# Kernel tuning notes

Measured on AMD Instinct MI355X. Metric: run time of the kernel, lower is better.

## Reference

```python
import jax, jax.numpy as jnp
import numpy as np

OUT_H, OUT_W = 7, 7
SPATIAL_SCALE = 0.0625
SAMPLING_RATIO = 2  # fixed sampling grid (> 0 branch in the original)


def setup_inputs() -> dict:
    key = jax.random.key(0)
    k1, k2, k3, k4, k5 = jax.random.split(key, 5)
    B, C, H, W = 2, 256, 200, 200
    R = 512
    x = jax.random.normal(k1, (B, C, H, W), dtype=jnp.float32)
    img = W / SPATIAL_SCALE  # 3200 px image coordinates
    b = jax.random.randint(k2, (R,), 0, B).astype(jnp.float32)
    x1 = jax.random.uniform(k3, (R,), minval=0.0, maxval=img * 0.8)
    y1 = jax.random.uniform(k4, (R,), minval=0.0, maxval=img * 0.8)
    wh = jax.random.uniform(k5, (R, 2), minval=32.0, maxval=img * 0.2)
    rois = jnp.stack([b, x1, y1, x1 + wh[:, 0], y1 + wh[:, 1]], axis=1).astype(jnp.float32)
    return {"input": x, "rois": rois}


def _axis_coords(start, bin_size, pooled, sr):
    # start: [R]; returns sample coordinates [R, pooled*sr]
    p = jnp.arange(pooled, dtype=jnp.float32)
    i = jnp.arange(sr, dtype=jnp.float32)
    c = (start[:, None, None]
         + p[None, :, None] * bin_size[:, None, None]
         + (i[None, None, :] + 0.5) * bin_size[:, None, None] / sr)
    return c.reshape(start.shape[0], pooled * sr)


def _interp_axis(c, size):
    # per-axis bilinear pieces; c: [R, G]
    valid = (c >= -1.0) & (c <= size)
    cc = jnp.maximum(c, 0.0)
    lo = jnp.floor(cc)
    at_edge = lo >= size - 1
    lo_i = jnp.minimum(lo, size - 1).astype(jnp.int32)
    hi_i = jnp.minimum(lo_i + 1, size - 1)
    frac = jnp.where(at_edge, 0.0, cc - lo)  # l (weight toward hi)
    return lo_i, hi_i, frac, valid


def reference(input, rois):
    R = rois.shape[0]
    B, C, H, W = input.shape
    b = rois[:, 0].astype(jnp.int32)
    x1 = rois[:, 1] * SPATIAL_SCALE
    y1 = rois[:, 2] * SPATIAL_SCALE
    x2 = rois[:, 3] * SPATIAL_SCALE
    y2 = rois[:, 4] * SPATIAL_SCALE
    roi_w = jnp.maximum(x2 - x1, 1.0)
    roi_h = jnp.maximum(y2 - y1, 1.0)
    bin_w = roi_w / OUT_W
    bin_h = roi_h / OUT_H

    ys = _axis_coords(y1, bin_h, OUT_H, SAMPLING_RATIO)  # [R, Yg]
    xs = _axis_coords(x1, bin_w, OUT_W, SAMPLING_RATIO)  # [R, Xg]
    yl, yh, ly, vy = _interp_axis(ys, H)
    xl, xh, lx, vx = _interp_axis(xs, W)
    hy, hx = 1.0 - ly, 1.0 - lx

    bb = b[:, None, None]
    # advanced indexing -> [R, Yg, Xg, C]
    v1 = input[bb, :, yl[:, :, None], xl[:, None, :]]
    v2 = input[bb, :, yl[:, :, None], xh[:, None, :]]
    v3 = input[bb, :, yh[:, :, None], xl[:, None, :]]
    v4 = input[bb, :, yh[:, :, None], xh[:, None, :]]

    w1 = (hy[:, :, None] * hx[:, None, :])[..., None]
    w2 = (hy[:, :, None] * lx[:, None, :])[..., None]
    w3 = (ly[:, :, None] * hx[:, None, :])[..., None]
    w4 = (ly[:, :, None] * lx[:, None, :])[..., None]

    val = w1 * v1 + w2 * v2 + w3 * v3 + w4 * v4
    val = val * (vy[:, :, None] & vx[:, None, :])[..., None]

    S = SAMPLING_RATIO
    val = val.reshape(R, OUT_H, S, OUT_W, S, C).sum(axis=(2, 4)) / (S * S)
    return jnp.transpose(val, (0, 3, 1, 2))  # [R, C, OUT_H, OUT_W]
```

## Files before the change

### kernel.cpp

```cpp
#include <hip/hip_runtime.h>
#include <hip/hip_fp16.h>


#define B_  2
#define C_  256
#define H_  200
#define W_  200
#define R_  512
#define HW_ (H_ * W_)
#define TOTAL_ (B_ * C_ * HW_)
#define BUF_ 1600
#define G_   8

#define HDR_BYTES_  (R_ * 8 * 4)
#define META_BYTES_ (R_ * 4 * 64 * 16)
#define PERM_BYTES_ (R_ * 4)
#define WS_NEED_    (HDR_BYTES_ + META_BYTES_ + PERM_BYTES_)

typedef __attribute__((address_space(3))) unsigned int lds_u32;
typedef const __attribute__((address_space(1))) unsigned int glb_u32;

__device__ __forceinline__ float sample_coord(float start, float bin, int p, int i) {
    return start + (float)p * bin + ((float)i + 0.5f) * bin * 0.5f;
}
__device__ __forceinline__ int lo_clamped(float v, int size) {
    return (int)fminf(floorf(fmaxf(v, 0.0f)), (float)(size - 1));
}
__device__ __forceinline__ unsigned int pack_h2(float a, float b) {
    unsigned short ua = __half_as_ushort(__float2half(a));
    unsigned short ub = __half_as_ushort(__float2half(b));
    return (unsigned int)ua | ((unsigned int)ub << 16);
}
__device__ __forceinline__ float h2f_lo(unsigned int u) {
    return __half2float(__ushort_as_half((unsigned short)(u & 0xffffu)));
}
__device__ __forceinline__ float h2f_hi(unsigned int u) {
    return __half2float(__ushort_as_half((unsigned short)(u >> 16)));
}

__global__ __launch_bounds__(512) void roialign_sort(
    const float* __restrict__ rois, int* __restrict__ perm) {
    __shared__ unsigned int keys[R_];
    int t = threadIdx.x;

    float bf = rois[t * 5 + 0];
    float cx = (rois[t * 5 + 1] + rois[t * 5 + 3]) * 0.5f * 0.0625f;
    float cy = (rois[t * 5 + 2] + rois[t * 5 + 4]) * 0.5f * 0.0625f;
    int bi = (int)bf;
    int ys = min(3, max(0, (int)(cy * (4.0f / 200.0f))));
    int xq = min(255, max(0, (int)(cx * (256.0f / 200.0f))));
    unsigned int key = ((unsigned int)bi << 10) | ((unsigned int)ys << 8) |
                       (unsigned int)xq;
    unsigned int mykey = (key << 9) | (unsigned int)t;
    keys[t] = mykey;
    __syncthreads();

    int rank = 0;
#pragma unroll 8
    for (int u = 0; u < R_; ++u)
        rank += (keys[u] < mykey) ? 1 : 0;
    perm[rank] = t;
}

__global__ __launch_bounds__(64) void roialign_meta(
    const float* __restrict__ rois, int* __restrict__ hdr, int4* __restrict__ meta) {
    int r = blockIdx.x;
    int lane = threadIdx.x;

    const float scale = 0.0625f;
    float bf = rois[r * 5 + 0];
    int   bi = (int)bf;
    float x1 = rois[r * 5 + 1] * scale;
    float y1 = rois[r * 5 + 2] * scale;
    float x2 = rois[r * 5 + 3] * scale;
    float y2 = rois[r * 5 + 4] * scale;
    float bin_w = fmaxf(x2 - x1, 1.0f) * (1.0f / 7.0f);
    float bin_h = fmaxf(y2 - y1, 1.0f) * (1.0f / 7.0f);

    int y0 = lo_clamped(sample_coord(y1, bin_h, 0, 0), H_);
    int yE = min(lo_clamped(sample_coord(y1, bin_h, 6, 1), H_) + 1, H_ - 1);
    int x0 = lo_clamped(sample_coord(x1, bin_w, 0, 0), W_);
    int xE = min(lo_clamped(sample_coord(x1, bin_w, 6, 1), W_) + 1, W_ - 1);
    int rows = yE - y0 + 1;
    int cols = xE - x0 + 1;
    int cols4 = (cols + 3) & ~3;
    if ((cols4 & 31) == 0) cols4 += 4;
    int   T = rows * cols4;
    int   nIter = (T + 255) >> 8;
    float recip = 1.0f / (float)cols4;

    if (lane == 0) {
        int* h = hdr + r * 8;
        h[0] = y0 * W_ + x0;
        h[1] = bi;
        h[2] = cols4;
        h[3] = T;
        h[4] = __float_as_int(recip);
        h[5] = nIter;
        h[6] = 0;
        h[7] = 0;
    }

    int4 o[4] = {{0,0,0,0},{0,0,0,0},{0,0,0,0},{0,0,0,0}};
    if (lane < 49) {
        int ph = lane / 7;
        int pw = lane % 7;

        int   rlo_b[2], rhi_b[2];
        float fy[2];
        bool  vy[2];
#pragma unroll
        for (int iy = 0; iy < 2; ++iy) {
            float y = sample_coord(y1, bin_h, ph, iy);
            vy[iy] = (y >= -1.0f) && (y <= (float)H_);
            float yc = fmaxf(y, 0.0f);
            float yl = floorf(yc);
            bool  edge = yl >= (float)(H_ - 1);
            int   lo = (int)fminf(yl, (float)(H_ - 1));
            int   hi = min(lo + 1, H_ - 1);
            fy[iy] = edge ? 0.0f : (yc - yl);
            rlo_b[iy] = (lo - y0) * cols4 * 4;
            rhi_b[iy] = (hi - y0) * cols4 * 4;
        }
        int   clo_b[2], chi_b[2];
        float fx[2];
        bool  vx[2];
#pragma unroll
        for (int ix = 0; ix < 2; ++ix) {
            float x = sample_coord(x1, bin_w, pw, ix);
            vx[ix] = (x >= -1.0f) && (x <= (float)W_);
            float xc = fmaxf(x, 0.0f);
            float xl = floorf(xc);
            bool  edge = xl >= (float)(W_ - 1);
            int   lo = (int)fminf(xl, (float)(W_ - 1));
            int   hi = min(lo + 1, W_ - 1);
            fx[ix] = edge ? 0.0f : (xc - xl);
            clo_b[ix] = (lo - x0) * 4;
            chi_b[ix] = (hi - x0) * 4;
        }
#pragma unroll
        for (int iy = 0; iy < 2; ++iy)
#pragma unroll
            for (int ix = 0; ix < 2; ++ix) {
                int s = iy * 2 + ix;
                float mk  = (vy[iy] && vx[ix]) ? 0.25f : 0.0f;
                float wy0 = (1.0f - fy[iy]) * mk;
                float wy1 = fy[iy] * mk;
                float wx0 = 1.0f - fx[ix];
                float wx1 = fx[ix];
                o[s].x = rlo_b[iy] | (rhi_b[iy] << 16);
                o[s].y = clo_b[ix] | (chi_b[ix] << 16);
                o[s].z = (int)pack_h2(wy0, wy1);
                o[s].w = (int)pack_h2(wx0, wx1);
            }
    }
#pragma unroll
    for (int s = 0; s < 4; ++s)
        meta[((r * 4 + s) * 64) + lane] = o[s];
}

template<int N> __device__ __forceinline__ void wait_vmcnt() {
    if constexpr (N == 0)      asm volatile("s_waitcnt vmcnt(0)" ::: "memory");
    else if constexpr (N == 1) asm volatile("s_waitcnt vmcnt(1)" ::: "memory");
    else if constexpr (N == 2) asm volatile("s_waitcnt vmcnt(2)" ::: "memory");
    else if constexpr (N == 3) asm volatile("s_waitcnt vmcnt(3)" ::: "memory");
    else if constexpr (N == 4) asm volatile("s_waitcnt vmcnt(4)" ::: "memory");
    else if constexpr (N == 5) asm volatile("s_waitcnt vmcnt(5)" ::: "memory");
    else if constexpr (N == 6) asm volatile("s_waitcnt vmcnt(6)" ::: "memory");
    else                       asm volatile("s_waitcnt vmcnt(7)" ::: "memory");
}

template<int NI>
__device__ __forceinline__ void body(
    const float* __restrict__ input, float* __restrict__ out,
    float* __restrict__ b0, float* __restrict__ b1,
    int lane, int srcbase, int cols4, float recip, int T,
    const int (&off)[16], const float (&wt)[16], int obase) {

    int e4 = lane << 2;

    int so[NI];
#pragma unroll
    for (int i = 0; i < NI; ++i) {
        int e = e4 + (i << 8);
        int row = (int)(((float)e + 0.5f) * recip);
        int col = e - row * cols4;
        so[i] = srcbase + row * W_ + col;
    }

    auto STAGE = [&](float* bp) {
#pragma unroll
        for (int i = 0; i < NI; ++i) {
            if (e4 + (i << 8) < T) {
                int g = min(so[i], TOTAL_ - 4);
                __builtin_amdgcn_global_load_lds((glb_u32*)(input + g),
                                                 (lds_u32*)(bp + (i << 8)), 16, 0, 0);
            }
            so[i] += HW_;
        }
    };

    STAGE(b0);
    STAGE(b1);

    float accs[G_];
#pragma unroll
    for (int k = 0; k < G_; ++k) {
        if (k < G_ - 1) wait_vmcnt<NI>(); else wait_vmcnt<0>();
        float* bp = (k & 1) ? b1 : b0;
        const char* bb = (const char*)bp;
        float a = 0.0f;
#pragma unroll
        for (int s = 0; s < 4; ++s) {
            float v1 = *(const float*)(bb + off[4*s+0]);
            float v2 = *(const float*)(bb + off[4*s+1]);
            float v3 = *(const float*)(bb + off[4*s+2]);
            float v4 = *(const float*)(bb + off[4*s+3]);
            a += wt[4*s+0] * (wt[4*s+2] * v1 + wt[4*s+3] * v2)
               + wt[4*s+1] * (wt[4*s+2] * v3 + wt[4*s+3] * v4);
        }
        accs[k] = a;
        if (k < G_ - 2) {
            asm volatile("s_waitcnt lgkmcnt(0)" ::: "memory");
            __builtin_amdgcn_sched_barrier(0);
            STAGE(bp);
        }
    }

    if (lane < 49) {
#pragma unroll
        for (int k = 0; k < G_; ++k)
            out[obase + k * 49] = accs[k];
    }
}

__global__ __launch_bounds__(128) void roialign_main(
    const float* __restrict__ input, const int* __restrict__ hdr,
    const int4* __restrict__ meta, const int* __restrict__ perm,
    float* __restrict__ out) {
    __shared__ float lds[2][2][BUF_];
    int tid  = threadIdx.x;
    int lane = tid & 63;
    int w    = tid >> 6;
    int bidx = blockIdx.x;

    int xcd    = bidx & 7;
    int ixn    = bidx >> 3;
    int rank   = (xcd << 6) | (ixn & 63);
    int cgpair = ixn >> 6;
    int r      = perm[rank];
    int cg     = (cgpair << 1) | w;
    int c0     = cg << 3;

    int4 m[4];
#pragma unroll
    for (int s = 0; s < 4; ++s)
        m[s] = meta[(((r << 2) + s) << 6) + lane];

    const int* h = hdr + (r << 3);
    int   rel_off = h[0];
    int   bi      = h[1];
    int   cols4   = h[2];
    int   T       = h[3];
    float recip   = __int_as_float(h[4]);
    int   nIter   = __builtin_amdgcn_readfirstlane(h[5]);

    int   off[16];
    float wt[16];
#pragma unroll
    for (int s = 0; s < 4; ++s) {
        unsigned int d0 = (unsigned int)m[s].x;
        unsigned int d1 = (unsigned int)m[s].y;
        int rlo = (int)(d0 & 0xffffu), rhi = (int)(d0 >> 16);
        int clo = (int)(d1 & 0xffffu), chi = (int)(d1 >> 16);
        off[4*s+0] = rlo + clo;
        off[4*s+1] = rlo + chi;
        off[4*s+2] = rhi + clo;
        off[4*s+3] = rhi + chi;
        unsigned int d2 = (unsigned int)m[s].z;
        unsigned int d3 = (unsigned int)m[s].w;
        wt[4*s+0] = h2f_lo(d2);
        wt[4*s+1] = h2f_hi(d2);
        wt[4*s+2] = h2f_lo(d3);
        wt[4*s+3] = h2f_hi(d3);
    }

    int srcbase = (bi * C_ + c0) * HW_ + rel_off;
    int obase   = (r * C_ + c0) * 49 + lane;
    float* b0 = lds[w][0];
    float* b1 = lds[w][1];

    switch (nIter) {
        case 1: body<1>(input, out, b0, b1, lane, srcbase, cols4, recip, T, off, wt, obase); break;
        case 2: body<2>(input, out, b0, b1, lane, srcbase, cols4, recip, T, off, wt, obase); break;
        case 3: body<3>(input, out, b0, b1, lane, srcbase, cols4, recip, T, off, wt, obase); break;
        case 4: body<4>(input, out, b0, b1, lane, srcbase, cols4, recip, T, off, wt, obase); break;
        case 5: body<5>(input, out, b0, b1, lane, srcbase, cols4, recip, T, off, wt, obase); break;
        case 6: body<6>(input, out, b0, b1, lane, srcbase, cols4, recip, T, off, wt, obase); break;
        default: body<7>(input, out, b0, b1, lane, srcbase, cols4, recip, T, off, wt, obase); break;
    }
}

#define RMAX_   41
#define STRIDE_ 42

__global__ __launch_bounds__(128) void roialign_fallback(
    const float* __restrict__ input,
    const float* __restrict__ rois,
    float* __restrict__ out) {
    __shared__ float lds[2][RMAX_ * STRIDE_];

    int lane = threadIdx.x & 63;
    int wv   = threadIdx.x >> 6;
    int bidx = blockIdx.x;
    int r = bidx >> 7;
    int c = ((bidx & 127) << 1) | wv;

    const float scale = 0.0625f;
    float bf = rois[r * 5 + 0];
    int   bi = (int)bf;
    float x1 = rois[r * 5 + 1] * scale;
    float y1 = rois[r * 5 + 2] * scale;
    float x2 = rois[r * 5 + 3] * scale;
    float y2 = rois[r * 5 + 4] * scale;
    float bin_w = fmaxf(x2 - x1, 1.0f) * (1.0f / 7.0f);
    float bin_h = fmaxf(y2 - y1, 1.0f) * (1.0f / 7.0f);

    int y0 = lo_clamped(sample_coord(y1, bin_h, 0, 0), H_);
    int x0 = lo_clamped(sample_coord(x1, bin_w, 0, 0), W_);
    int yE = min(lo_clamped(sample_coord(y1, bin_h, 6, 1), H_) + 1, H_ - 1);
    int xE = min(lo_clamped(sample_coord(x1, bin_w, 6, 1), W_) + 1, W_ - 1);
    int rows = min(yE - y0 + 1, RMAX_);
    int cols = min(xE - x0 + 1, RMAX_);

    const float* plane = input + ((size_t)bi * C_ + c) * HW_;
    float* myl = lds[wv];
    for (int rr = 0; rr < rows; ++rr) {
        lds_u32* dst = (lds_u32*)(myl + rr * STRIDE_);
        const float* src = plane + (y0 + rr) * W_ + x0 + lane;
        if (lane < cols)
            __builtin_amdgcn_global_load_lds((glb_u32*)src, dst, 4, 0, 0);
    }
    asm volatile("s_waitcnt vmcnt(0)" ::: "memory");
    __builtin_amdgcn_sched_barrier(0);

    if (lane < 49) {
        int ph = lane / 7;
        int pw = lane % 7;
        int   ry[2][2];
        float fy[2];
        bool  vy[2];
#pragma unroll
        for (int iy = 0; iy < 2; ++iy) {
            float y = sample_coord(y1, bin_h, ph, iy);
            vy[iy] = (y >= -1.0f) && (y <= (float)H_);
            float yc = fmaxf(y, 0.0f);
            float yl = floorf(yc);
            bool  edge = yl >= (float)(H_ - 1);
            int   lo = (int)fminf(yl, (float)(H_ - 1));
            int   hi = min(lo + 1, H_ - 1);
            fy[iy] = edge ? 0.0f : (yc - yl);
            ry[iy][0] = (lo - y0) * STRIDE_;
            ry[iy][1] = (hi - y0) * STRIDE_;
        }
        int   rxl[2], rxh[2];
        float fx[2];
        bool  vx[2];
#pragma unroll
        for (int ix = 0; ix < 2; ++ix) {
            float x = sample_coord(x1, bin_w, pw, ix);
            vx[ix] = (x >= -1.0f) && (x <= (float)W_);
            float xc = fmaxf(x, 0.0f);
            float xl = floorf(xc);
            bool  edge = xl >= (float)(W_ - 1);
            int   lo = (int)fminf(xl, (float)(W_ - 1));
            int   hi = min(lo + 1, W_ - 1);
            fx[ix] = edge ? 0.0f : (xc - xl);
            rxl[ix] = lo - x0;
            rxh[ix] = hi - x0;
        }
        float acc = 0.0f;
#pragma unroll
        for (int iy = 0; iy < 2; ++iy) {
            float lyw = fy[iy], hyw = 1.0f - lyw;
#pragma unroll
            for (int ix = 0; ix < 2; ++ix) {
                float lxw = fx[ix], hxw = 1.0f - lxw;
                float msk = (vy[iy] && vx[ix]) ? 1.0f : 0.0f;
                float v1 = myl[ry[iy][0] + rxl[ix]];
                float v2 = myl[ry[iy][0] + rxh[ix]];
                float v3 = myl[ry[iy][1] + rxl[ix]];
                float v4 = myl[ry[iy][1] + rxh[ix]];
                acc += msk * (hyw * hxw * v1 + hyw * lxw * v2 +
                              lyw * hxw * v3 + lyw * lxw * v4);
            }
        }
        out[(r * C_ + c) * 49 + lane] = acc * 0.25f;
    }
}

extern "C" void kernel_launch(void* const* d_in, const int* in_sizes, int n_in,
                              void* d_out, int out_size, void* d_ws, size_t ws_size,
                              hipStream_t stream) {
    const float* input = (const float*)d_in[0];
    const float* rois  = (const float*)d_in[1];
    float* out = (float*)d_out;

    if (ws_size >= (size_t)WS_NEED_) {
        int*  hdr  = (int*)d_ws;
        int4* meta = (int4*)((char*)d_ws + HDR_BYTES_);
        int*  perm = (int*)((char*)d_ws + HDR_BYTES_ + META_BYTES_);
        roialign_sort<<<1, R_, 0, stream>>>(rois, perm);
        roialign_meta<<<R_, 64, 0, stream>>>(rois, hdr, meta);
        roialign_main<<<R_ * 16, 128, 0, stream>>>(input, hdr, meta, perm, out);
    } else {
        roialign_fallback<<<R_ * (C_ / 2), 128, 0, stream>>>(input, rois, out);
    }
}
```

Baseline: 53.34 us.

## Replace LDS-staged ROI tile copy with direct float2 global gathers

The main kernel no longer copies each ROI's bounding tile of every channel into LDS with async global-to-LDS loads. Each lane now gathers its four bilinear corners straight from global memory as two float2 loads per sample, with register double-buffering across the 8 channels. Edge columns are handled with a select flag. Blocks grow to 4 waves covering 32 channels each, launched as half as many blocks. This drops the tile-staging traffic and the LDS reads, in exchange for uncoalesced per-lane gathers that depend on the cache.

```diff
diff --git a/kernel.cpp b/kernel.cpp
--- a/kernel.cpp
+++ b/kernel.cpp
@@ -8,8 +8,6 @@
 #define W_  200
 #define R_  512
 #define HW_ (H_ * W_)
-#define TOTAL_ (B_ * C_ * HW_)
-#define BUF_ 1600
 #define G_   8
 
 #define HDR_BYTES_  (R_ * 8 * 4)
@@ -77,28 +75,9 @@
     float bin_w = fmaxf(x2 - x1, 1.0f) * (1.0f / 7.0f);
     float bin_h = fmaxf(y2 - y1, 1.0f) * (1.0f / 7.0f);
 
-    int y0 = lo_clamped(sample_coord(y1, bin_h, 0, 0), H_);
-    int yE = min(lo_clamped(sample_coord(y1, bin_h, 6, 1), H_) + 1, H_ - 1);
-    int x0 = lo_clamped(sample_coord(x1, bin_w, 0, 0), W_);
-    int xE = min(lo_clamped(sample_coord(x1, bin_w, 6, 1), W_) + 1, W_ - 1);
-    int rows = yE - y0 + 1;
-    int cols = xE - x0 + 1;
-    int cols4 = (cols + 3) & ~3;
-    if ((cols4 & 31) == 0) cols4 += 4;
-    int   T = rows * cols4;
-    int   nIter = (T + 255) >> 8;
-    float recip = 1.0f / (float)cols4;
-
     if (lane == 0) {
         int* h = hdr + r * 8;
-        h[0] = y0 * W_ + x0;
         h[1] = bi;
-        h[2] = cols4;
-        h[3] = T;
-        h[4] = __float_as_int(recip);
-        h[5] = nIter;
-        h[6] = 0;
-        h[7] = 0;
     }
 
     int4 o[4] = {{0,0,0,0},{0,0,0,0},{0,0,0,0},{0,0,0,0}};
@@ -106,7 +85,7 @@
         int ph = lane / 7;
         int pw = lane % 7;
 
-        int   rlo_b[2], rhi_b[2];
+        int   ylo[2], dyW[2];
         float fy[2];
         bool  vy[2];
 #pragma unroll
@@ -119,10 +98,11 @@
             int   lo = (int)fminf(yl, (float)(H_ - 1));
             int   hi = min(lo + 1, H_ - 1);
             fy[iy] = edge ? 0.0f : (yc - yl);
-            rlo_b[iy] = (lo - y0) * cols4 * 4;
-            rhi_b[iy] = (hi - y0) * cols4 * 4;
-        }
-        int   clo_b[2], chi_b[2];
+            ylo[iy] = lo;
+            dyW[iy] = (hi - lo) * W_;
+        }
+        int   xo[2];
+        bool  sx[2];
         float fx[2];
         bool  vx[2];
 #pragma unroll
@@ -133,10 +113,9 @@
             float xl = floorf(xc);
             bool  edge = xl >= (float)(W_ - 1);
             int   lo = (int)fminf(xl, (float)(W_ - 1));
-            int   hi = min(lo + 1, W_ - 1);
             fx[ix] = edge ? 0.0f : (xc - xl);
-            clo_b[ix] = (lo - x0) * 4;
-            chi_b[ix] = (hi - x0) * 4;
+            sx[ix] = (lo == W_ - 1);
+            xo[ix] = min(lo, W_ - 2);
         }
 #pragma unroll
         for (int iy = 0; iy < 2; ++iy)
@@ -148,8 +127,8 @@
                 float wy1 = fy[iy] * mk;
                 float wx0 = 1.0f - fx[ix];
                 float wx1 = fx[ix];
-                o[s].x = rlo_b[iy] | (rhi_b[iy] << 16);
-                o[s].y = clo_b[ix] | (chi_b[ix] << 16);
+                o[s].x = ylo[iy] * W_ + xo[ix];
+                o[s].y = dyW[iy] | (sx[ix] ? (1 << 30) : 0);
                 o[s].z = (int)pack_h2(wy0, wy1);
                 o[s].w = (int)pack_h2(wx0, wx1);
             }
@@ -159,124 +138,60 @@
         meta[((r * 4 + s) * 64) + lane] = o[s];
 }
 
-template<int N> __device__ __forceinline__ void wait_vmcnt() {
-    if constexpr (N == 0)      asm volatile("s_waitcnt vmcnt(0)" ::: "memory");
-    else if constexpr (N == 1) asm volatile("s_waitcnt vmcnt(1)" ::: "memory");
-    else if constexpr (N == 2) asm volatile("s_waitcnt vmcnt(2)" ::: "memory");
-    else if constexpr (N == 3) asm volatile("s_waitcnt vmcnt(3)" ::: "memory");
-    else if constexpr (N == 4) asm volatile("s_waitcnt vmcnt(4)" ::: "memory");
-    else if constexpr (N == 5) asm volatile("s_waitcnt vmcnt(5)" ::: "memory");
-    else if constexpr (N == 6) asm volatile("s_waitcnt vmcnt(6)" ::: "memory");
-    else                       asm volatile("s_waitcnt vmcnt(7)" ::: "memory");
-}
-
-template<int NI>
-__device__ __forceinline__ void body(
-    const float* __restrict__ input, float* __restrict__ out,
-    float* __restrict__ b0, float* __restrict__ b1,
-    int lane, int srcbase, int cols4, float recip, int T,
-    const int (&off)[16], const float (&wt)[16], int obase) {
-
-    int e4 = lane << 2;
-
-    int so[NI];
-#pragma unroll
-    for (int i = 0; i < NI; ++i) {
-        int e = e4 + (i << 8);
-        int row = (int)(((float)e + 0.5f) * recip);
-        int col = e - row * cols4;
-        so[i] = srcbase + row * W_ + col;
-    }
-
-    auto STAGE = [&](float* bp) {
-#pragma unroll
-        for (int i = 0; i < NI; ++i) {
-            if (e4 + (i << 8) < T) {
-                int g = min(so[i], TOTAL_ - 4);
-                __builtin_amdgcn_global_load_lds((glb_u32*)(input + g),
-                                                 (lds_u32*)(bp + (i << 8)), 16, 0, 0);
-            }
-            so[i] += HW_;
-        }
-    };
-
-    STAGE(b0);
-    STAGE(b1);
-
-    float accs[G_];
-#pragma unroll
-    for (int k = 0; k < G_; ++k) {
-        if (k < G_ - 1) wait_vmcnt<NI>(); else wait_vmcnt<0>();
-        float* bp = (k & 1) ? b1 : b0;
-        const char* bb = (const char*)bp;
-        float a = 0.0f;
-#pragma unroll
-        for (int s = 0; s < 4; ++s) {
-            float v1 = *(const float*)(bb + off[4*s+0]);
-            float v2 = *(const float*)(bb + off[4*s+1]);
-            float v3 = *(const float*)(bb + off[4*s+2]);
-            float v4 = *(const float*)(bb + off[4*s+3]);
-            a += wt[4*s+0] * (wt[4*s+2] * v1 + wt[4*s+3] * v2)
-               + wt[4*s+1] * (wt[4*s+2] * v3 + wt[4*s+3] * v4);
-        }
-        accs[k] = a;
-        if (k < G_ - 2) {
-            asm volatile("s_waitcnt lgkmcnt(0)" ::: "memory");
-            __builtin_amdgcn_sched_barrier(0);
-            STAGE(bp);
-        }
-    }
-
-    if (lane < 49) {
-#pragma unroll
-        for (int k = 0; k < G_; ++k)
-            out[obase + k * 49] = accs[k];
-    }
-}
-
-__global__ __launch_bounds__(128) void roialign_main(
+__device__ __forceinline__ void load_ch(
+    const float* __restrict__ plane, const int4 (&m)[4], float2 (&d)[8]) {
+#pragma unroll
+    for (int s = 0; s < 4; ++s) {
+        int base2 = m[s].x;
+        int dyW   = m[s].y & 0xffff;
+        d[s * 2 + 0] = *(const float2*)(plane + base2);
+        d[s * 2 + 1] = *(const float2*)(plane + base2 + dyW);
+    }
+}
+
+__device__ __forceinline__ float compute_ch(
+    const float2 (&d)[8], const int4 (&m)[4], const float (&wt)[16]) {
+    float a = 0.0f;
+#pragma unroll
+    for (int s = 0; s < 4; ++s) {
+        bool sx = (m[s].y >> 30) & 1;
+        float2 A = d[s * 2 + 0];
+        float2 Bv = d[s * 2 + 1];
+        float v1 = sx ? A.y : A.x;
+        float v3 = sx ? Bv.y : Bv.x;
+        a += wt[4*s+0] * (wt[4*s+2] * v1 + wt[4*s+3] * A.y)
+           + wt[4*s+1] * (wt[4*s+2] * v3 + wt[4*s+3] * Bv.y);
+    }
+    return a;
+}
+
+__global__ __launch_bounds__(256) void roialign_gather(
     const float* __restrict__ input, const int* __restrict__ hdr,
     const int4* __restrict__ meta, const int* __restrict__ perm,
     float* __restrict__ out) {
-    __shared__ float lds[2][2][BUF_];
     int tid  = threadIdx.x;
     int lane = tid & 63;
     int w    = tid >> 6;
     int bidx = blockIdx.x;
 
-    int xcd    = bidx & 7;
-    int ixn    = bidx >> 3;
-    int rank   = (xcd << 6) | (ixn & 63);
-    int cgpair = ixn >> 6;
-    int r      = perm[rank];
-    int cg     = (cgpair << 1) | w;
-    int c0     = cg << 3;
+    int xcd  = bidx & 7;
+    int ixn  = bidx >> 3;
+    int rank = (xcd << 6) | (ixn & 63);
+    int bg   = ixn >> 6;
+    int r    = perm[rank];
+    int cg   = (bg << 2) | w;
+    int c0   = cg << 3;
 
     int4 m[4];
 #pragma unroll
     for (int s = 0; s < 4; ++s)
         m[s] = meta[(((r << 2) + s) << 6) + lane];
 
-    const int* h = hdr + (r << 3);
-    int   rel_off = h[0];
-    int   bi      = h[1];
-    int   cols4   = h[2];
-    int   T       = h[3];
-    float recip   = __int_as_float(h[4]);
-    int   nIter   = __builtin_amdgcn_readfirstlane(h[5]);
-
-    int   off[16];
+    int bi = hdr[(r << 3) + 1];
+
     float wt[16];
 #pragma unroll
     for (int s = 0; s < 4; ++s) {
-        unsigned int d0 = (unsigned int)m[s].x;
-        unsigned int d1 = (unsigned int)m[s].y;
-        int rlo = (int)(d0 & 0xffffu), rhi = (int)(d0 >> 16);
-        int clo = (int)(d1 & 0xffffu), chi = (int)(d1 >> 16);
-        off[4*s+0] = rlo + clo;
-        off[4*s+1] = rlo + chi;
-        off[4*s+2] = rhi + clo;
-        off[4*s+3] = rhi + chi;
         unsigned int d2 = (unsigned int)m[s].z;
         unsigned int d3 = (unsigned int)m[s].w;
         wt[4*s+0] = h2f_lo(d2);
@@ -285,19 +200,23 @@
         wt[4*s+3] = h2f_hi(d3);
     }
 
-    int srcbase = (bi * C_ + c0) * HW_ + rel_off;
-    int obase   = (r * C_ + c0) * 49 + lane;
-    float* b0 = lds[w][0];
-    float* b1 = lds[w][1];
-
-    switch (nIter) {
-        case 1: body<1>(input, out, b0, b1, lane, srcbase, cols4, recip, T, off, wt, obase); break;
-        case 2: body<2>(input, out, b0, b1, lane, srcbase, cols4, recip, T, off, wt, obase); break;
-        case 3: body<3>(input, out, b0, b1, lane, srcbase, cols4, recip, T, off, wt, obase); break;
-        case 4: body<4>(input, out, b0, b1, lane, srcbase, cols4, recip, T, off, wt, obase); break;
-        case 5: body<5>(input, out, b0, b1, lane, srcbase, cols4, recip, T, off, wt, obase); break;
-        case 6: body<6>(input, out, b0, b1, lane, srcbase, cols4, recip, T, off, wt, obase); break;
-        default: body<7>(input, out, b0, b1, lane, srcbase, cols4, recip, T, off, wt, obase); break;
+    const float* plane0 = input + ((size_t)bi * C_ + c0) * HW_;
+    int obase = (r * C_ + c0) * 49 + lane;
+
+    float2 dA[8], dB[8];
+    float accs[G_];
+    load_ch(plane0, m, dA);
+#pragma unroll
+    for (int k = 0; k < G_; ++k) {
+        if (k + 1 < G_)
+            load_ch(plane0 + (k + 1) * HW_, m, (k & 1) ? dA : dB);
+        accs[k] = compute_ch((k & 1) ? dB : dA, m, wt);
+    }
+
+    if (lane < 49) {
+#pragma unroll
+        for (int k = 0; k < G_; ++k)
+            out[obase + k * 49] = accs[k];
     }
 }
 
@@ -412,7 +331,7 @@
         int*  perm = (int*)((char*)d_ws + HDR_BYTES_ + META_BYTES_);
         roialign_sort<<<1, R_, 0, stream>>>(rois, perm);
         roialign_meta<<<R_, 64, 0, stream>>>(rois, hdr, meta);
-        roialign_main<<<R_ * 16, 128, 0, stream>>>(input, hdr, meta, perm, out);
+        roialign_gather<<<R_ * 8, 256, 0, stream>>>(input, hdr, meta, perm, out);
     } else {
         roialign_fallback<<<R_ * (C_ / 2), 128, 0, stream>>>(input, rois, out);
     }
```

Result: slower. 63.66 us (+19.4%).
